# Performance work log

Hardware: AMD Instinct MI355X
Metric: run time of the kernel (lower is better)

The kernel has to match this reference:

```python
import jax, jax.numpy as jnp
import numpy as np

N_NODES = 50000
N_EDGES = 800000
D_FEAT = 64          # per-node feature dim
HIDDEN = 128         # fc1 output dim; fc1 input = 2*D_FEAT


def setup_inputs() -> dict:
    key = jax.random.key(0)
    k1, k2, k3 = jax.random.split(key, 3)
    x = jax.random.normal(k1, (N_NODES, D_FEAT), dtype=jnp.float32)
    edge_index = jax.random.randint(k2, (2, N_EDGES), 0, N_NODES, dtype=jnp.int64)
    # fc1: Linear(2*D_FEAT, HIDDEN); torch Linear weight is [out, in]
    W = jax.random.normal(k3, (HIDDEN, 2 * D_FEAT), dtype=jnp.float32) * (1.0 / np.sqrt(2 * D_FEAT))
    b = jnp.zeros((HIDDEN,), dtype=jnp.float32)
    return {"x": x, "edge_index": edge_index, "W": W, "b": b}


def reference(x, edge_index, W, b):
    # Gather source-node features along edges, sum-scatter to destinations.
    src, dst = edge_index[0], edge_index[1]
    gathered = x[src]  # [E, D_FEAT] -- dominant memory traffic
    neigh = jax.ops.segment_sum(gathered, dst, num_segments=x.shape[0])  # [N, D_FEAT]
    # Concat self features with aggregated neighbor features, then Linear+ReLU.
    h = jnp.concatenate([x, neigh], axis=-1)          # [N, 2*D_FEAT]
    out = jax.nn.relu(h @ W.T + b)                    # [N, HIDDEN]
    return out
```

## Files before the change

### kernel.cpp

```cpp
#include <hip/hip_runtime.h>

#define N_NODES 50000
#define N_EDGES 800000
#define DFEAT 64
#define HID 128
#define NBKT 16
#define NPB1 3200
#define SLOTS 112
#define CAPB (782 * SLOTS)
#define SEGS 14
#define NRCH 56
#define SUBB 50
#define NSUB 800
#define CAP_S 1536
#define NSTR 66

#define XB_BLOCKS 3125
#define WB_BLOCKS 16
#define EB_BLOCKS 782

typedef __bf16 bf16x8 __attribute__((ext_vector_type(8)));
typedef float f32x4 __attribute__((ext_vector_type(4)));

__device__ inline unsigned short f2bf(float f) {
  unsigned u = __float_as_uint(f);
  return (unsigned short)((u + 0x7FFFu + ((u >> 16) & 1u)) >> 16);
}
__device__ inline float bf2f(unsigned short h) {
  return __uint_as_float(((unsigned)h) << 16);
}

__global__ __launch_bounds__(256) void k_prep(const float* __restrict__ x,
                                              const float* __restrict__ W,
                                              const int* __restrict__ ei,
                                              unsigned short* __restrict__ xb,
                                              unsigned short* __restrict__ Wb,
                                              int* __restrict__ subcnt,
                                              int* __restrict__ pcnt,
                                              unsigned int* __restrict__ coarse) {
  int bid = blockIdx.x;
  if (bid < XB_BLOCKS) {
    int t = bid * 256 + threadIdx.x;
    float4 v = *(const float4*)&x[t * 4];
    ushort4 o = {f2bf(v.x), f2bf(v.y), f2bf(v.z), f2bf(v.w)};
    *(ushort4*)&xb[t * 4] = o;
    return;
  }
  bid -= XB_BLOCKS;
  if (bid < WB_BLOCKS) {
    int t = bid * 256 + threadIdx.x;
    float4 v = *(const float4*)&W[t * 4];
    ushort4 o = {f2bf(v.x), f2bf(v.y), f2bf(v.z), f2bf(v.w)};
    *(ushort4*)&Wb[t * 4] = o;
    int z = bid * 50 + threadIdx.x;
    if (threadIdx.x < 50 && z < NSUB) subcnt[z] = 0;
    return;
  }
  bid -= WB_BLOCKS;
  __shared__ int lcnt[NBKT];
  const int tid = threadIdx.x;
  if (tid < NBKT) lcnt[tid] = 0;
  __syncthreads();

  int e0 = (bid * 256 + tid) * 4;
  bool valid = e0 < N_EDGES;
  if (valid) {
    int4 s4 = *(const int4*)&ei[e0];
    int4 d4 = *(const int4*)&ei[N_EDGES + e0];
    int ss[4] = {s4.x, s4.y, s4.z, s4.w};
    int dd[4] = {d4.x, d4.y, d4.z, d4.w};
#pragma unroll
    for (int i = 0; i < 4; ++i) {
      int bkt = dd[i] / NPB1;
      int rank = atomicAdd(&lcnt[bkt], 1);
      if (rank < SLOTS)
        coarse[(size_t)bkt * CAPB + bid * SLOTS + rank] =
            ((unsigned)dd[i] << 16) | (unsigned)ss[i];
    }
  }
  __syncthreads();
  if (tid < NBKT) {
    int c = lcnt[tid];
    pcnt[bid * NBKT + tid] = c < SLOTS ? c : SLOTS;
  }
}

__global__ __launch_bounds__(256) void k_refine(const unsigned int* __restrict__ coarse,
                                                const int* __restrict__ pcnt,
                                                int* __restrict__ subcnt,
                                                unsigned int* __restrict__ sub) {
  __shared__ int lcnt[SUBB];
  __shared__ int lbase[SUBB];
  __shared__ int scnt[SEGS];
  const int tid = threadIdx.x;
  const int b = blockIdx.x / NRCH;
  const int c = blockIdx.x % NRCH;

  if (tid < SUBB) lcnt[tid] = 0;
  if (tid < SEGS) {
    int seg = c * SEGS + tid;
    scnt[tid] = (seg < EB_BLOCKS) ? pcnt[seg * NBKT + b] : 0;
  }
  __syncthreads();

  unsigned p[7];
  int sl[7], rk[7];
  bool v[7];
#pragma unroll
  for (int j = 0; j < 7; ++j) {
    int idx = j * 256 + tid;
    v[j] = false;
    if (idx < SEGS * SLOTS) {
      int seg = idx / SLOTS;
      int off = idx % SLOTS;
      if (off < scnt[seg]) {
        p[j] = coarse[(size_t)b * CAPB + (c * SEGS + seg) * SLOTS + off];
        sl[j] = ((int)(p[j] >> 16) >> 6) - b * SUBB;
        rk[j] = atomicAdd(&lcnt[sl[j]], 1);
        v[j] = true;
      }
    }
  }
  __syncthreads();
  if (tid < SUBB) lbase[tid] = atomicAdd(&subcnt[b * SUBB + tid], lcnt[tid]);
  __syncthreads();
#pragma unroll
  for (int j = 0; j < 7; ++j) {
    if (v[j]) {
      int pos = lbase[sl[j]] + rk[j];
      if (pos < CAP_S)
        sub[(size_t)(b * SUBB + sl[j]) * CAP_S + pos] =
            ((p[j] & 0x3f0000u)) | (p[j] & 0xffffu);
    }
  }
}

__global__ __launch_bounds__(1024) void k_gnn(const unsigned short* __restrict__ xb,
                                              const unsigned short* __restrict__ Wb,
                                              const int* __restrict__ subcnt,
                                              const unsigned int* __restrict__ sub,
                                              const float* __restrict__ bv,
                                              float* __restrict__ out) {
  __shared__ unsigned int q[CAP_S];
  __shared__ unsigned int sq[CAP_S];
  __shared__ unsigned int ns_u[32 * NSTR];
  __shared__ int lcnt[64];
  __shared__ int lbase[65];

  const int tid = threadIdx.x;
  const int sb = blockIdx.x;
  const int nb = sb * 64;

  if (tid < 64) lcnt[tid] = 0;

  int cnt = subcnt[sb];
  cnt = cnt < CAP_S ? cnt : CAP_S;
  const unsigned int* qb = &sub[(size_t)sb * CAP_S];
  for (int i = tid; i < cnt; i += 1024) q[i] = qb[i];
  __syncthreads();

  int myrank[2], myidx[2], nloc = 0;
  for (int i = tid; i < cnt; i += 1024) {
    int rel = (int)(q[i] >> 16);
    myrank[nloc] = atomicAdd(&lcnt[rel], 1);
    myidx[nloc] = i;
    ++nloc;
  }
  __syncthreads();
  if (tid < 64) {
    int v = lcnt[tid];
    int inc = v;
#pragma unroll
    for (int o = 1; o < 64; o <<= 1) {
      int u = __shfl_up(inc, o);
      if (tid >= o) inc += u;
    }
    lbase[tid] = inc - v;
    if (tid == 63) lbase[64] = inc;
  }
  __syncthreads();
  for (int k = 0; k < nloc; ++k) {
    unsigned e = q[myidx[k]];
    sq[lbase[e >> 16] + myrank[k]] = e;
  }
  __syncthreads();

  const int wave = tid >> 6;
  const int lane = tid & 63;
  const int half = lane >> 5;
  const int l31 = lane & 31;
  const unsigned int* xu = (const unsigned int*)xb;

#pragma unroll
  for (int i2 = 0; i2 < 4; ++i2) {
    int n = wave * 4 + i2;
    int beg = lbase[n], end = lbase[n + 1];
    float s0x = 0.f, s0y = 0.f, s1x = 0.f, s1y = 0.f,
          s2x = 0.f, s2y = 0.f, s3x = 0.f, s3y = 0.f;
    int j = beg + half;
    for (; j + 6 < end; j += 8) {
      unsigned e0 = sq[j], e1 = sq[j + 2], e2 = sq[j + 4], e3 = sq[j + 6];
      unsigned v0 = xu[(e0 & 0xffffu) * 32 + l31];
      unsigned v1 = xu[(e1 & 0xffffu) * 32 + l31];
      unsigned v2 = xu[(e2 & 0xffffu) * 32 + l31];
      unsigned v3 = xu[(e3 & 0xffffu) * 32 + l31];
      s0x += bf2f((unsigned short)(v0 & 0xffffu)); s0y += bf2f((unsigned short)(v0 >> 16));
      s1x += bf2f((unsigned short)(v1 & 0xffffu)); s1y += bf2f((unsigned short)(v1 >> 16));
      s2x += bf2f((unsigned short)(v2 & 0xffffu)); s2y += bf2f((unsigned short)(v2 >> 16));
      s3x += bf2f((unsigned short)(v3 & 0xffffu)); s3y += bf2f((unsigned short)(v3 >> 16));
    }
    for (; j < end; j += 2) {
      unsigned e = sq[j];
      unsigned v = xu[(e & 0xffffu) * 32 + l31];
      s0x += bf2f((unsigned short)(v & 0xffffu));
      s0y += bf2f((unsigned short)(v >> 16));
    }
    float sx = (s0x + s1x) + (s2x + s3x);
    float sy = (s0y + s1y) + (s2y + s3y);
    sx += __shfl_xor(sx, 32);
    sy += __shfl_xor(sy, 32);
    if (half == 0)
      ns_u[l31 * NSTR + n] = (unsigned)f2bf(sx) | ((unsigned)f2bf(sy) << 16);
  }
  __syncthreads();

  const int g = wave & 3;
  const int o = wave >> 2;
  const int l15 = lane & 15;
  const int quad = lane >> 4;
  const int node0 = nb + g * 16;

  int anode = node0 + l15;
  if (anode >= N_NODES) anode = N_NODES - 1;
  const unsigned short* hx = xb + (size_t)anode * DFEAT;

  bf16x8 fa0 = *(const bf16x8*)(hx + quad * 8);
  bf16x8 fa1 = *(const bf16x8*)(hx + 32 + quad * 8);
  bf16x8 fa2, fa3;
  {
    int m = g * 16 + l15;
    union { unsigned u[4]; bf16x8 v; } c2, c3;
#pragma unroll
    for (int i = 0; i < 4; ++i) {
      c2.u[i] = ns_u[(quad * 4 + i) * NSTR + m];
      c3.u[i] = ns_u[(16 + quad * 4 + i) * NSTR + m];
    }
    fa2 = c2.v;
    fa3 = c3.v;
  }

  f32x4 accr[2];
#pragma unroll
  for (int t = 0; t < 2; ++t) accr[t] = (f32x4){0.f, 0.f, 0.f, 0.f};

#pragma unroll
  for (int t = 0; t < 2; ++t) {
    int nt = o * 2 + t;
    const unsigned short* wr = Wb + (size_t)(nt * 16 + l15) * (2 * DFEAT) + quad * 8;
    bf16x8 b0 = *(const bf16x8*)(wr);
    bf16x8 b1 = *(const bf16x8*)(wr + 32);
    bf16x8 b2 = *(const bf16x8*)(wr + 64);
    bf16x8 b3 = *(const bf16x8*)(wr + 96);
    accr[t] = __builtin_amdgcn_mfma_f32_16x16x32_bf16(fa0, b0, accr[t], 0, 0, 0);
    accr[t] = __builtin_amdgcn_mfma_f32_16x16x32_bf16(fa1, b1, accr[t], 0, 0, 0);
    accr[t] = __builtin_amdgcn_mfma_f32_16x16x32_bf16(fa2, b2, accr[t], 0, 0, 0);
    accr[t] = __builtin_amdgcn_mfma_f32_16x16x32_bf16(fa3, b3, accr[t], 0, 0, 0);
  }

#pragma unroll
  for (int t = 0; t < 2; ++t) {
    int nt = o * 2 + t;
    float bias = bv[nt * 16 + l15];
#pragma unroll
    for (int r = 0; r < 4; ++r) {
      int node = node0 + quad * 4 + r;
      if (node < N_NODES) {
        float v = accr[t][r] + bias;
        out[(size_t)node * HID + nt * 16 + l15] = v > 0.f ? v : 0.f;
      }
    }
  }
}

extern "C" void kernel_launch(void* const* d_in, const int* in_sizes, int n_in,
                              void* d_out, int out_size, void* d_ws, size_t ws_size,
                              hipStream_t stream) {
  const float* x = (const float*)d_in[0];
  const int* ei = (const int*)d_in[1];
  const float* W = (const float*)d_in[2];
  const float* b = (const float*)d_in[3];
  float* out = (float*)d_out;

  char* ws = (char*)d_ws;
  int* subcnt          = (int*)ws;            ws += 3328;
  int* pcnt            = (int*)ws;            ws += (size_t)EB_BLOCKS * NBKT * 4;
  unsigned int* coarse = (unsigned int*)ws;   ws += (size_t)NBKT * CAPB * 4;
  unsigned int* sub    = (unsigned int*)ws;   ws += (size_t)NSUB * CAP_S * 4;
  unsigned short* xb   = (unsigned short*)ws; ws += (size_t)N_NODES * DFEAT * 2;
  unsigned short* Wb   = (unsigned short*)ws; ws += (size_t)HID * 2 * DFEAT * 2;

  k_prep<<<XB_BLOCKS + WB_BLOCKS + EB_BLOCKS, 256, 0, stream>>>(
      x, W, ei, xb, Wb, subcnt, pcnt, coarse);
  k_refine<<<NBKT * NRCH, 256, 0, stream>>>(coarse, pcnt, subcnt, sub);
  k_gnn<<<(N_NODES + 63) / 64, 1024, 0, stream>>>(xb, Wb, subcnt, sub, b, out);
}
```

Before: 127.1 us.

## Bucket edges directly per 64-node block and drop the refine pass

Edges are binned straight into 782 per-block buckets, each with small fixed-width segments headed by a count, so the separate refine kernel and its global atomics go away. The GNN kernel compacts its bucket's segments into shared memory itself. The gather now has each lane load 8 bytes and four edges run in parallel per wave, with cross-lane reductions at the end. The risk is segment overflow: with 15 slots per segment, edges beyond that are silently dropped, and scanning mostly empty segments adds read traffic.

```diff
diff --git a/kernel.cpp b/kernel.cpp
--- a/kernel.cpp
+++ b/kernel.cpp
@@ -4,20 +4,15 @@
 #define N_EDGES 800000
 #define DFEAT 64
 #define HID 128
-#define NBKT 16
-#define NPB1 3200
-#define SLOTS 112
-#define CAPB (782 * SLOTS)
-#define SEGS 14
-#define NRCH 56
-#define SUBB 50
-#define NSUB 800
+#define NBKT 782
+#define NSEG 391
+#define SEGW 16
 #define CAP_S 1536
 #define NSTR 66
 
-#define XB_BLOCKS 3125
-#define WB_BLOCKS 16
-#define EB_BLOCKS 782
+#define XB2 1563
+#define WB2 8
+#define EB2 391
 
 typedef __bf16 bf16x8 __attribute__((ext_vector_type(8)));
 typedef float f32x4 __attribute__((ext_vector_type(4)));
@@ -30,134 +25,104 @@
   return __uint_as_float(((unsigned)h) << 16);
 }
 
-__global__ __launch_bounds__(256) void k_prep(const float* __restrict__ x,
+__global__ __launch_bounds__(512) void k_prep(const float* __restrict__ x,
                                               const float* __restrict__ W,
                                               const int* __restrict__ ei,
                                               unsigned short* __restrict__ xb,
                                               unsigned short* __restrict__ Wb,
-                                              int* __restrict__ subcnt,
-                                              int* __restrict__ pcnt,
                                               unsigned int* __restrict__ coarse) {
   int bid = blockIdx.x;
-  if (bid < XB_BLOCKS) {
-    int t = bid * 256 + threadIdx.x;
-    float4 v = *(const float4*)&x[t * 4];
-    ushort4 o = {f2bf(v.x), f2bf(v.y), f2bf(v.z), f2bf(v.w)};
-    *(ushort4*)&xb[t * 4] = o;
+  const int tid = threadIdx.x;
+  if (bid < XB2) {
+    int t = bid * 512 + tid;
+    if (t < N_NODES * DFEAT / 4) {
+      float4 v = *(const float4*)&x[t * 4];
+      ushort4 o = {f2bf(v.x), f2bf(v.y), f2bf(v.z), f2bf(v.w)};
+      *(ushort4*)&xb[t * 4] = o;
+    }
     return;
   }
-  bid -= XB_BLOCKS;
-  if (bid < WB_BLOCKS) {
-    int t = bid * 256 + threadIdx.x;
+  bid -= XB2;
+  if (bid < WB2) {
+    int t = bid * 512 + tid;
     float4 v = *(const float4*)&W[t * 4];
     ushort4 o = {f2bf(v.x), f2bf(v.y), f2bf(v.z), f2bf(v.w)};
     *(ushort4*)&Wb[t * 4] = o;
-    int z = bid * 50 + threadIdx.x;
-    if (threadIdx.x < 50 && z < NSUB) subcnt[z] = 0;
     return;
   }
-  bid -= WB_BLOCKS;
+  bid -= WB2;
   __shared__ int lcnt[NBKT];
-  const int tid = threadIdx.x;
-  if (tid < NBKT) lcnt[tid] = 0;
-  __syncthreads();
-
-  int e0 = (bid * 256 + tid) * 4;
-  bool valid = e0 < N_EDGES;
-  if (valid) {
+  for (int i = tid; i < NBKT; i += 512) lcnt[i] = 0;
+  __syncthreads();
+
+  int e0 = (bid * 512 + tid) * 4;
+  if (e0 < N_EDGES) {
     int4 s4 = *(const int4*)&ei[e0];
     int4 d4 = *(const int4*)&ei[N_EDGES + e0];
     int ss[4] = {s4.x, s4.y, s4.z, s4.w};
     int dd[4] = {d4.x, d4.y, d4.z, d4.w};
 #pragma unroll
     for (int i = 0; i < 4; ++i) {
-      int bkt = dd[i] / NPB1;
+      int bkt = dd[i] >> 6;
       int rank = atomicAdd(&lcnt[bkt], 1);
-      if (rank < SLOTS)
-        coarse[(size_t)bkt * CAPB + bid * SLOTS + rank] =
+      if (rank < SEGW - 1)
+        coarse[(size_t)bkt * (NSEG * SEGW) + bid * SEGW + 1 + rank] =
             ((unsigned)dd[i] << 16) | (unsigned)ss[i];
     }
   }
   __syncthreads();
-  if (tid < NBKT) {
-    int c = lcnt[tid];
-    pcnt[bid * NBKT + tid] = c < SLOTS ? c : SLOTS;
-  }
-}
-
-__global__ __launch_bounds__(256) void k_refine(const unsigned int* __restrict__ coarse,
-                                                const int* __restrict__ pcnt,
-                                                int* __restrict__ subcnt,
-                                                unsigned int* __restrict__ sub) {
-  __shared__ int lcnt[SUBB];
-  __shared__ int lbase[SUBB];
-  __shared__ int scnt[SEGS];
-  const int tid = threadIdx.x;
-  const int b = blockIdx.x / NRCH;
-  const int c = blockIdx.x % NRCH;
-
-  if (tid < SUBB) lcnt[tid] = 0;
-  if (tid < SEGS) {
-    int seg = c * SEGS + tid;
-    scnt[tid] = (seg < EB_BLOCKS) ? pcnt[seg * NBKT + b] : 0;
-  }
-  __syncthreads();
-
-  unsigned p[7];
-  int sl[7], rk[7];
-  bool v[7];
-#pragma unroll
-  for (int j = 0; j < 7; ++j) {
-    int idx = j * 256 + tid;
-    v[j] = false;
-    if (idx < SEGS * SLOTS) {
-      int seg = idx / SLOTS;
-      int off = idx % SLOTS;
-      if (off < scnt[seg]) {
-        p[j] = coarse[(size_t)b * CAPB + (c * SEGS + seg) * SLOTS + off];
-        sl[j] = ((int)(p[j] >> 16) >> 6) - b * SUBB;
-        rk[j] = atomicAdd(&lcnt[sl[j]], 1);
-        v[j] = true;
-      }
-    }
-  }
-  __syncthreads();
-  if (tid < SUBB) lbase[tid] = atomicAdd(&subcnt[b * SUBB + tid], lcnt[tid]);
-  __syncthreads();
-#pragma unroll
-  for (int j = 0; j < 7; ++j) {
-    if (v[j]) {
-      int pos = lbase[sl[j]] + rk[j];
-      if (pos < CAP_S)
-        sub[(size_t)(b * SUBB + sl[j]) * CAP_S + pos] =
-            ((p[j] & 0x3f0000u)) | (p[j] & 0xffffu);
-    }
+  for (int i = tid; i < NBKT; i += 512) {
+    int c = lcnt[i];
+    coarse[(size_t)i * (NSEG * SEGW) + bid * SEGW] =
+        (unsigned)(c < SEGW - 1 ? c : SEGW - 1);
   }
 }
 
 __global__ __launch_bounds__(1024) void k_gnn(const unsigned short* __restrict__ xb,
                                               const unsigned short* __restrict__ Wb,
-                                              const int* __restrict__ subcnt,
-                                              const unsigned int* __restrict__ sub,
+                                              const unsigned int* __restrict__ coarse,
                                               const float* __restrict__ bv,
                                               float* __restrict__ out) {
   __shared__ unsigned int q[CAP_S];
   __shared__ unsigned int sq[CAP_S];
   __shared__ unsigned int ns_u[32 * NSTR];
+  __shared__ int scnt[NSEG];
   __shared__ int lcnt[64];
   __shared__ int lbase[65];
+  __shared__ int qn;
 
   const int tid = threadIdx.x;
-  const int sb = blockIdx.x;
-  const int nb = sb * 64;
+  const int b = blockIdx.x;
+  const int nb = b * 64;
+  const unsigned int* base = coarse + (size_t)b * (NSEG * SEGW);
 
   if (tid < 64) lcnt[tid] = 0;
-
-  int cnt = subcnt[sb];
-  cnt = cnt < CAP_S ? cnt : CAP_S;
-  const unsigned int* qb = &sub[(size_t)sb * CAP_S];
-  for (int i = tid; i < cnt; i += 1024) q[i] = qb[i];
-  __syncthreads();
+  if (tid == 0) qn = 0;
+  for (int i = tid; i < NSEG; i += 1024) {
+    int c = (int)base[i * SEGW];
+    scnt[i] = c < SEGW - 1 ? c : SEGW - 1;
+  }
+  __syncthreads();
+
+  const int NU4 = NSEG * SEGW / 4;
+  for (int i = tid; i < NU4; i += 1024) {
+    uint4 w = ((const uint4*)base)[i];
+    int seg = i >> 2;
+    int wi = (i & 3) * 4;
+    int cnt = scnt[seg];
+    unsigned e[4] = {w.x, w.y, w.z, w.w};
+#pragma unroll
+    for (int k = 0; k < 4; ++k) {
+      int widx = wi + k;
+      if (widx >= 1 && widx <= cnt) {
+        int pos = atomicAdd(&qn, 1);
+        if (pos < CAP_S) q[pos] = e[k] & 0x003fffffu;
+      }
+    }
+  }
+  __syncthreads();
+
+  int cnt = qn < CAP_S ? qn : CAP_S;
 
   int myrank[2], myidx[2], nloc = 0;
   for (int i = tid; i < cnt; i += 1024) {
@@ -187,40 +152,41 @@
 
   const int wave = tid >> 6;
   const int lane = tid & 63;
-  const int half = lane >> 5;
-  const int l31 = lane & 31;
-  const unsigned int* xu = (const unsigned int*)xb;
+  const int eslot = lane >> 4;
+  const int c = lane & 15;
+  const uint2* xu2 = (const uint2*)xb;
 
 #pragma unroll
   for (int i2 = 0; i2 < 4; ++i2) {
     int n = wave * 4 + i2;
     int beg = lbase[n], end = lbase[n + 1];
-    float s0x = 0.f, s0y = 0.f, s1x = 0.f, s1y = 0.f,
-          s2x = 0.f, s2y = 0.f, s3x = 0.f, s3y = 0.f;
-    int j = beg + half;
-    for (; j + 6 < end; j += 8) {
-      unsigned e0 = sq[j], e1 = sq[j + 2], e2 = sq[j + 4], e3 = sq[j + 6];
-      unsigned v0 = xu[(e0 & 0xffffu) * 32 + l31];
-      unsigned v1 = xu[(e1 & 0xffffu) * 32 + l31];
-      unsigned v2 = xu[(e2 & 0xffffu) * 32 + l31];
-      unsigned v3 = xu[(e3 & 0xffffu) * 32 + l31];
-      s0x += bf2f((unsigned short)(v0 & 0xffffu)); s0y += bf2f((unsigned short)(v0 >> 16));
-      s1x += bf2f((unsigned short)(v1 & 0xffffu)); s1y += bf2f((unsigned short)(v1 >> 16));
-      s2x += bf2f((unsigned short)(v2 & 0xffffu)); s2y += bf2f((unsigned short)(v2 >> 16));
-      s3x += bf2f((unsigned short)(v3 & 0xffffu)); s3y += bf2f((unsigned short)(v3 >> 16));
-    }
-    for (; j < end; j += 2) {
+    float f0 = 0.f, f1 = 0.f, f2 = 0.f, f3 = 0.f;
+    float g0 = 0.f, g1 = 0.f, g2 = 0.f, g3 = 0.f;
+    int j = beg + eslot;
+    for (; j + 4 < end; j += 8) {
+      unsigned e0 = sq[j], e1 = sq[j + 4];
+      uint2 v0 = xu2[(e0 & 0xffffu) * 16 + c];
+      uint2 v1 = xu2[(e1 & 0xffffu) * 16 + c];
+      f0 += bf2f((unsigned short)(v0.x & 0xffffu)); f1 += bf2f((unsigned short)(v0.x >> 16));
+      f2 += bf2f((unsigned short)(v0.y & 0xffffu)); f3 += bf2f((unsigned short)(v0.y >> 16));
+      g0 += bf2f((unsigned short)(v1.x & 0xffffu)); g1 += bf2f((unsigned short)(v1.x >> 16));
+      g2 += bf2f((unsigned short)(v1.y & 0xffffu)); g3 += bf2f((unsigned short)(v1.y >> 16));
+    }
+    for (; j < end; j += 4) {
       unsigned e = sq[j];
-      unsigned v = xu[(e & 0xffffu) * 32 + l31];
-      s0x += bf2f((unsigned short)(v & 0xffffu));
-      s0y += bf2f((unsigned short)(v >> 16));
-    }
-    float sx = (s0x + s1x) + (s2x + s3x);
-    float sy = (s0y + s1y) + (s2y + s3y);
-    sx += __shfl_xor(sx, 32);
-    sy += __shfl_xor(sy, 32);
-    if (half == 0)
-      ns_u[l31 * NSTR + n] = (unsigned)f2bf(sx) | ((unsigned)f2bf(sy) << 16);
+      uint2 v = xu2[(e & 0xffffu) * 16 + c];
+      f0 += bf2f((unsigned short)(v.x & 0xffffu)); f1 += bf2f((unsigned short)(v.x >> 16));
+      f2 += bf2f((unsigned short)(v.y & 0xffffu)); f3 += bf2f((unsigned short)(v.y >> 16));
+    }
+    f0 += g0; f1 += g1; f2 += g2; f3 += g3;
+    f0 += __shfl_xor(f0, 16); f0 += __shfl_xor(f0, 32);
+    f1 += __shfl_xor(f1, 16); f1 += __shfl_xor(f1, 32);
+    f2 += __shfl_xor(f2, 16); f2 += __shfl_xor(f2, 32);
+    f3 += __shfl_xor(f3, 16); f3 += __shfl_xor(f3, 32);
+    if (eslot == 0) {
+      ns_u[(2 * c) * NSTR + n] = (unsigned)f2bf(f0) | ((unsigned)f2bf(f1) << 16);
+      ns_u[(2 * c + 1) * NSTR + n] = (unsigned)f2bf(f2) | ((unsigned)f2bf(f3) << 16);
+    }
   }
   __syncthreads();
 
@@ -292,15 +258,10 @@
   float* out = (float*)d_out;
 
   char* ws = (char*)d_ws;
-  int* subcnt          = (int*)ws;            ws += 3328;
-  int* pcnt            = (int*)ws;            ws += (size_t)EB_BLOCKS * NBKT * 4;
-  unsigned int* coarse = (unsigned int*)ws;   ws += (size_t)NBKT * CAPB * 4;
-  unsigned int* sub    = (unsigned int*)ws;   ws += (size_t)NSUB * CAP_S * 4;
+  unsigned int* coarse = (unsigned int*)ws;   ws += (size_t)NBKT * NSEG * SEGW * 4;
   unsigned short* xb   = (unsigned short*)ws; ws += (size_t)N_NODES * DFEAT * 2;
   unsigned short* Wb   = (unsigned short*)ws; ws += (size_t)HID * 2 * DFEAT * 2;
 
-  k_prep<<<XB_BLOCKS + WB_BLOCKS + EB_BLOCKS, 256, 0, stream>>>(
-      x, W, ei, xb, Wb, subcnt, pcnt, coarse);
-  k_refine<<<NBKT * NRCH, 256, 0, stream>>>(coarse, pcnt, subcnt, sub);
-  k_gnn<<<(N_NODES + 63) / 64, 1024, 0, stream>>>(xb, Wb, subcnt, sub, b, out);
-}
+  k_prep<<<XB2 + WB2 + EB2, 512, 0, stream>>>(x, W, ei, xb, Wb, coarse);
+  k_gnn<<<NBKT, 1024, 0, stream>>>(xb, Wb, coarse, b, out);
+}
```

Result: no change. 126.7 us (-0.3%).
